# Kernel optimization log

Measured on AMD Instinct MI355X. Metric: run time of the kernel, lower is better.

## Reference

```python
import jax, jax.numpy as jnp
import numpy as np

N = 100000   # nodes
E = 1600000  # edges (avg degree 16)
F = 128      # num_node_features
H = 128      # hid_size
G = 512      # num graphs in batch
C = 10       # num_classes
D = 32       # graph_degree_distribution.shape[1]
BN_EPS = 1e-5


def setup_inputs() -> dict:
    key = jax.random.key(0)
    ks = jax.random.split(key, 16)
    p = lambda k, shp: jax.random.normal(k, shp, jnp.float32) * 0.02
    x = jax.random.normal(ks[0], (N, F), jnp.float32)
    edge_index = jax.random.randint(ks[1], (2, E), 0, N)
    batch = jnp.sort(jax.random.randint(ks[2], (N,), 0, G))
    degree = jax.random.uniform(ks[3], (N,), jnp.float32) * 10.0
    return dict(
        x=x, edge_index=edge_index, batch=batch, degree=degree,
        eps1=jnp.zeros(()), W1a=p(ks[4], (F, H)), b1a=jnp.zeros(H), W1b=p(ks[5], (H, H)), b1b=jnp.zeros(H),
        g1=jnp.ones(H), be1=jnp.zeros(H),
        eps2=jnp.zeros(()), W2a=p(ks[6], (H, H)), b2a=jnp.zeros(H), W2b=p(ks[7], (H, H)), b2b=jnp.zeros(H),
        g2=jnp.ones(H), be2=jnp.zeros(H),
        Wlin1=p(ks[8], (H, H)), blin1=jnp.zeros(H),
        Wlin2=p(ks[9], (H, C)), blin2=jnp.zeros(C),
        Wlin4=p(ks[10], (H, D)), blin4=jnp.zeros(D),
        Wloss=p(ks[11], (H, 1)), bloss=jnp.zeros(1),
    )


def gin_conv(x, src, dst, eps, Wa, ba, Wb, bb, gamma, beta):
    # GINConv: MLP((1+eps)*x_i + sum_{j->i} x_j); MLP = Lin-ReLU-Lin-ReLU-BN
    agg = jax.ops.segment_sum(x[src], dst, num_segments=x.shape[0])  # [N,F] gather-scatter
    h = (1.0 + eps) * x + agg
    h = jax.nn.relu(h @ Wa + ba)
    h = jax.nn.relu(h @ Wb + bb)
    mu = h.mean(0)
    var = h.var(0)  # biased var, training-mode BN
    return gamma * (h - mu) * jax.lax.rsqrt(var + BN_EPS) + beta


def reference(x, edge_index, batch, degree,
              eps1, W1a, b1a, W1b, b1b, g1, be1,
              eps2, W2a, b2a, W2b, b2b, g2, be2,
              Wlin1, blin1, Wlin2, blin2, Wlin4, blin4, Wloss, bloss):
    src, dst = edge_index[0], edge_index[1]
    h = gin_conv(x, src, dst, eps1, W1a, b1a, W1b, b1b, g1, be1)
    h = gin_conv(h, src, dst, eps2, W2a, b2a, W2b, b2b, g2, be2)
    mse_x = h @ Wloss + bloss                       # [N,1]
    mse_loss = jnp.mean((mse_x - degree[:, None]) ** 2)
    # global_mean_pool over graphs
    sums = jax.ops.segment_sum(h, batch, num_segments=G)
    cnts = jax.ops.segment_sum(jnp.ones((h.shape[0], 1), h.dtype), batch, num_segments=G)
    g = sums / jnp.maximum(cnts, 1.0)               # [G,H]
    z = jax.nn.relu(g @ Wlin1 + blin1)              # dropout inert (eval)
    result1 = jax.nn.log_softmax(z @ Wlin2 + blin2, axis=-1)  # [G,C]
    result3 = z @ Wlin4 + blin4                      # [G,D]
    return result1, result3, mse_loss
```

## Files before the change

kernel.cpp:

```cpp
#include <hip/hip_runtime.h>
#include <hip/hip_bf16.h>

#define HF 128
#define BSH 8
#define BSZ 256
#define NBMAX 1024
#define FCAP 8192
#define HB 512

typedef __attribute__((ext_vector_type(8))) short bf16x8;
typedef __attribute__((ext_vector_type(4))) float f32x4;
typedef __attribute__((ext_vector_type(2))) float f32x2;

__device__ inline float bflo(unsigned u) { return __uint_as_float(u << 16); }
__device__ inline float bfhi(unsigned u) { return __uint_as_float(u & 0xffff0000u); }
__device__ inline unsigned short f2bf(float f) {
    unsigned u = __float_as_uint(f);
    unsigned r = (u + 0x7fffu + ((u >> 16) & 1u)) >> 16;
    return (unsigned short)r;
}
__device__ inline unsigned pack2(float a, float b) {
    return (unsigned)f2bf(a) | ((unsigned)f2bf(b) << 16);
}
__device__ inline uint2 pk8_fp8(const float* v) {
    int a = __builtin_amdgcn_cvt_pk_fp8_f32(v[0], v[1], 0, 0);
    a = __builtin_amdgcn_cvt_pk_fp8_f32(v[2], v[3], a, 1);
    int b = __builtin_amdgcn_cvt_pk_fp8_f32(v[4], v[5], 0, 0);
    b = __builtin_amdgcn_cvt_pk_fp8_f32(v[6], v[7], b, 1);
    uint2 r; r.x = (unsigned)a; r.y = (unsigned)b;
    return r;
}

__global__ __launch_bounds__(256) void init_all(
    const float* __restrict__ x, unsigned short* __restrict__ xb,
    unsigned char* __restrict__ x8, int castBlk, int nchunks,
    const float* __restrict__ w0, const float* __restrict__ w1,
    const float* __restrict__ w2, const float* __restrict__ w3,
    unsigned short* __restrict__ WtAll,
    const int* __restrict__ dst, int* __restrict__ bpart, int E, int chunkH,
    const int* __restrict__ batch, int* __restrict__ gstart, int N, int Gn, int nBlocks,
    float* __restrict__ Szero, float* __restrict__ outm)
{
    __shared__ int lh[NBMAX];
    int b = blockIdx.x;
    int t = threadIdx.x;
    if (b < castBlk) {
        int i = b * 256 + t;
        if (i < nchunks) {
            float4 a = ((const float4*)x)[2 * i];
            float4 c = ((const float4*)x)[2 * i + 1];
            uint4 o;
            o.x = pack2(a.x, a.y); o.y = pack2(a.z, a.w);
            o.z = pack2(c.x, c.y); o.w = pack2(c.z, c.w);
            ((uint4*)xb)[i] = o;
            float v[8] = {a.x, a.y, a.z, a.w, c.x, c.y, c.z, c.w};
            ((uint2*)x8)[i] = pk8_fp8(v);
        }
        return;
    }
    b -= castBlk;
    if (b < 4) {
        const float* W = (b == 0) ? w0 : (b == 1) ? w1 : (b == 2) ? w2 : w3;
        unsigned short* O = WtAll + b * 16384;
        for (int idx = t; idx < 16384; idx += 256) {
            int j    = idx & 7;
            int lane = (idx >> 3) & 63;
            int fk   = idx >> 9;
            int kk = fk & 3, nt = fk >> 2;
            int m = lane & 15, quad = lane >> 4;
            int ncol = nt * 16 + m;
            int krow = kk * 32 + quad * 8 + j;
            O[idx] = f2bf(W[krow * 128 + ncol]);
        }
        return;
    }
    b -= 4;
    if (b < HB) {
        int NBl = (N + BSZ - 1) >> BSH;
        for (int i = t; i < NBl; i += 256) lh[i] = 0;
        __syncthreads();
        int beg = b * chunkH;
        int end = min(E, beg + chunkH);
        for (int e = beg + t; e < end; e += 256)
            atomicAdd(&lh[dst[e] >> BSH], 1);
        __syncthreads();
        for (int i = t; i < NBl; i += 256) bpart[i * HB + b] = lh[i];
        return;
    }
    b -= HB;
    if (b < nBlocks) {
        int i = b * 256 + t;
        if (i >= N) return;
        int bi = batch[i];
        int bp = (i == 0) ? -1 : batch[i - 1];
        for (int g = bp + 1; g <= bi; g++) gstart[g] = i;
        if (i == N - 1)
            for (int g = bi + 1; g <= Gn; g++) gstart[g] = N;
        return;
    }
    if (t < 2 * HF) { Szero[t] = 0.f; Szero[t + 2 * HF] = 0.f; }
    if (t == 0) outm[0] = 0.f;
}

__global__ void scanp(const int* __restrict__ bpart, int* __restrict__ boff,
                      int* __restrict__ bcur, int NB, int E)
{
    __shared__ int tot[NBMAX];
    __shared__ int part[256];
    int t = threadIdx.x;
    for (int i = t; i < NB; i += 256) {
        const int4* pp = (const int4*)(bpart + (size_t)i * HB);
        int run = 0;
#pragma unroll 4
        for (int b = 0; b < HB / 4; b++) {
            int4 v = pp[b];
            run += v.x + v.y + v.z + v.w;
        }
        tot[i] = run;
    }
    __syncthreads();
    int v[4];
    int s = 0;
#pragma unroll
    for (int i = 0; i < 4; i++) {
        int idx = t * 4 + i;
        v[i] = (idx < NB) ? tot[idx] : 0;
        s += v[i];
    }
    part[t] = s;
    __syncthreads();
    for (int o = 1; o < 256; o <<= 1) {
        int y = (t >= o) ? part[t - o] : 0;
        __syncthreads();
        part[t] += y;
        __syncthreads();
    }
    int base = part[t] - s;
#pragma unroll
    for (int i = 0; i < 4; i++) {
        int idx = t * 4 + i;
        if (idx < NB) { boff[idx] = base; bcur[idx] = base; base += v[i]; }
    }
    if (t == 0) boff[NB] = E;
}

__global__ __launch_bounds__(256) void bucket_bin(
    const int* __restrict__ src, const int* __restrict__ dst,
    int* __restrict__ bcur, unsigned* __restrict__ ebuf, int E, int NB, int chunkH)
{
    __shared__ int lh[NBMAX];
    int t = threadIdx.x;
    for (int i = t; i < NB; i += 256) lh[i] = 0;
    __syncthreads();
    int beg = blockIdx.x * chunkH;
    int end = min(E, beg + chunkH);
    for (int e = beg + t; e < end; e += 256)
        atomicAdd(&lh[dst[e] >> BSH], 1);
    __syncthreads();
    for (int i = t; i < NB; i += 256) {
        int c = lh[i];
        lh[i] = c ? atomicAdd(&bcur[i], c) : 0;
    }
    __syncthreads();
    for (int e = beg + t; e < end; e += 256) {
        int d = dst[e];
        int b = d >> BSH;
        int pos = atomicAdd(&lh[b], 1);
        ebuf[pos] = ((unsigned)src[e] << BSH) | (unsigned)(d & (BSZ - 1));
    }
}

__global__ __launch_bounds__(256) void bucket_fill(
    const unsigned* __restrict__ ebuf, const int* __restrict__ boff,
    int* __restrict__ off, int* __restrict__ esrc, int N, int NB, int E)
{
    __shared__ int deg[BSZ];
    __shared__ int pref[BSZ];
    __shared__ int lcur[BSZ];
    __shared__ int lsr[FCAP];
    int b = blockIdx.x;
    int t = threadIdx.x;
    int segBeg = boff[b], segEnd = boff[b + 1];
    int segLen = segEnd - segBeg;
    int node0 = b << BSH;
    deg[t] = 0;
    __syncthreads();
    for (int i = segBeg + t; i < segEnd; i += 256)
        atomicAdd(&deg[ebuf[i] & (BSZ - 1)], 1);
    __syncthreads();
    int dv = deg[t];
    pref[t] = dv;
    __syncthreads();
    for (int o = 1; o < 256; o <<= 1) {
        int y = (t >= o) ? pref[t - o] : 0;
        __syncthreads();
        pref[t] += y;
        __syncthreads();
    }
    int excl = pref[t] - dv;
    int node = node0 + t;
    if (node < N) off[node] = segBeg + excl;
    lcur[t] = excl;
    if (b == NB - 1 && t == 0) off[N] = E;
    __syncthreads();
    if (segLen <= FCAP) {
        for (int i = segBeg + t; i < segEnd; i += 256) {
            unsigned v = ebuf[i];
            int slot = atomicAdd(&lcur[v & (BSZ - 1)], 1);
            lsr[slot] = (int)(v >> BSH);
        }
        __syncthreads();
        for (int i = t; i < segLen; i += 256) esrc[segBeg + i] = lsr[i];
    } else {
        for (int i = segBeg + t; i < segEnd; i += 256) {
            unsigned v = ebuf[i];
            int slot = atomicAdd(&lcur[v & (BSZ - 1)], 1);
            esrc[segBeg + slot] = (int)(v >> BSH);
        }
    }
}

template <bool FOLD>
__global__ __launch_bounds__(256) void gather_u(
    const unsigned short* __restrict__ xb, const unsigned char* __restrict__ x8,
    const int* __restrict__ off, const int* __restrict__ esrc,
    const float* __restrict__ epsp,
    const float* __restrict__ S1, const float* __restrict__ S2,
    const float* __restrict__ gamma, const float* __restrict__ beta, float invN,
    unsigned short* __restrict__ Uo, int N)
{
    __shared__ float lsc[HF], lsh[HF];
    int tid = threadIdx.x;
    if (FOLD) {
        if (tid < HF) {
            float mu = S1[tid] * invN;
            float var = S2[tid] * invN - mu * mu;
            float rs = rsqrtf(var + 1e-5f);
            float sc = gamma[tid] * rs;
            lsc[tid] = sc;
            lsh[tid] = beta[tid] - mu * sc;
        }
        __syncthreads();
    }
    int lane16 = tid & 15;
    int node = (blockIdx.x * 256 + tid) >> 4;
    if (node >= N) return;
    int beg = off[node], end = off[node + 1];
    float acc[8] = {0.f, 0.f, 0.f, 0.f, 0.f, 0.f, 0.f, 0.f};
    for (int j0 = beg; j0 < end; j0 += 16) {
        int myidx = (j0 + lane16 < end) ? esrc[j0 + lane16] : 0;
        int cnt = min(16, end - j0);
        for (int t = 0; t < cnt; t++) {
            int s = __shfl(myidx, t, 16);
            uint2 p = *(const uint2*)(x8 + (size_t)s * HF + lane16 * 8);
            f32x2 f0 = __builtin_amdgcn_cvt_pk_f32_fp8((int)p.x, 0);
            f32x2 f1 = __builtin_amdgcn_cvt_pk_f32_fp8((int)p.x, 1);
            f32x2 f2 = __builtin_amdgcn_cvt_pk_f32_fp8((int)p.y, 0);
            f32x2 f3 = __builtin_amdgcn_cvt_pk_f32_fp8((int)p.y, 1);
            acc[0] += f0.x; acc[1] += f0.y;
            acc[2] += f1.x; acc[3] += f1.y;
            acc[4] += f2.x; acc[5] += f2.y;
            acc[6] += f3.x; acc[7] += f3.y;
        }
    }
    float ep = 1.0f + epsp[0];
    uint4 xx = *(const uint4*)(xb + (size_t)node * HF + lane16 * 8);
    acc[0] += ep * bflo(xx.x); acc[1] += ep * bfhi(xx.x);
    acc[2] += ep * bflo(xx.y); acc[3] += ep * bfhi(xx.y);
    acc[4] += ep * bflo(xx.z); acc[5] += ep * bfhi(xx.z);
    acc[6] += ep * bflo(xx.w); acc[7] += ep * bfhi(xx.w);
    if (FOLD) {
        float cf = ep + (float)(end - beg);
        const float4 s0 = *(const float4*)(&lsc[lane16 * 8]);
        const float4 s1 = *(const float4*)(&lsc[lane16 * 8 + 4]);
        const float4 h0 = *(const float4*)(&lsh[lane16 * 8]);
        const float4 h1 = *(const float4*)(&lsh[lane16 * 8 + 4]);
        acc[0] = acc[0] * s0.x + h0.x * cf; acc[1] = acc[1] * s0.y + h0.y * cf;
        acc[2] = acc[2] * s0.z + h0.z * cf; acc[3] = acc[3] * s0.w + h0.w * cf;
        acc[4] = acc[4] * s1.x + h1.x * cf; acc[5] = acc[5] * s1.y + h1.y * cf;
        acc[6] = acc[6] * s1.z + h1.z * cf; acc[7] = acc[7] * s1.w + h1.w * cf;
    }
    uint4 o;
    o.x = pack2(acc[0], acc[1]); o.y = pack2(acc[2], acc[3]);
    o.z = pack2(acc[4], acc[5]); o.w = pack2(acc[6], acc[7]);
    *(uint4*)(Uo + (size_t)node * HF + lane16 * 8) = o;
}

__global__ __launch_bounds__(256) void gemm2L(
    const unsigned short* __restrict__ U,
    const unsigned short* __restrict__ Wfa, const float* __restrict__ ba,
    const unsigned short* __restrict__ Wfb, const float* __restrict__ bb,
    unsigned short* __restrict__ out, unsigned char* __restrict__ out8,
    float* __restrict__ S1, float* __restrict__ S2, int n)
{
    __shared__ __align__(16) unsigned short lWa[16384];
    __shared__ __align__(16) unsigned short lWb[16384];
    __shared__ __align__(16) unsigned short lT[8192];
    int tid = threadIdx.x;
    int w = tid >> 6, lane = tid & 63;
    int m = lane & 15, quad = lane >> 4;

    for (int i = tid; i < 2048; i += 256) {
        ((uint4*)lWa)[i] = ((const uint4*)Wfa)[i];
        ((uint4*)lWb)[i] = ((const uint4*)Wfb)[i];
    }
    __syncthreads();

    float bav[8], bbv[8];
#pragma unroll
    for (int nt = 0; nt < 8; nt++) { bav[nt] = ba[nt * 16 + m]; bbv[nt] = bb[nt * 16 + m]; }

    unsigned short* lTw = lT + w * 2048;
    int swzA = (m & 7) << 3;

    float csA[8], cqA[8];
#pragma unroll
    for (int nt = 0; nt < 8; nt++) { csA[nt] = 0.f; cqA[nt] = 0.f; }

    int wid = (blockIdx.x << 2) | w;
    int nw = gridDim.x << 2;
    int ntiles = (n + 15) >> 4;

    bf16x8 aF[4];
    int tile = wid;
    if (tile < ntiles) {
        int ar = tile * 16 + m; if (ar >= n) ar = n - 1;
        const unsigned short* up = U + (size_t)ar * HF + quad * 8;
#pragma unroll
        for (int kk = 0; kk < 4; kk++) aF[kk] = *(const bf16x8*)(up + kk * 32);
    }

    for (; tile < ntiles; tile += nw) {
        bf16x8 aN[4];
        {
            int tn = tile + nw;
            int tl = (tn < ntiles) ? tn : tile;
            int ar = tl * 16 + m; if (ar >= n) ar = n - 1;
            const unsigned short* up = U + (size_t)ar * HF + quad * 8;
#pragma unroll
            for (int kk = 0; kk < 4; kk++) aN[kk] = *(const bf16x8*)(up + kk * 32);
        }

        f32x4 acc[8];
#pragma unroll
        for (int nt = 0; nt < 8; nt++) acc[nt] = (f32x4){0.f, 0.f, 0.f, 0.f};
#pragma unroll
        for (int nt = 0; nt < 8; nt++) {
#pragma unroll
            for (int kk = 0; kk < 4; kk++) {
                bf16x8 b = *(const bf16x8*)(&lWa[((((nt << 2) | kk) << 6) | lane) << 3]);
                acc[nt] = __builtin_amdgcn_mfma_f32_16x16x32_bf16(aF[kk], b, acc[nt], 0, 0, 0);
            }
        }
#pragma unroll
        for (int nt = 0; nt < 8; nt++) {
#pragma unroll
            for (int r = 0; r < 4; r++) {
                int row = (quad << 2) | r;
                lTw[(row << 7) | ((nt * 16 + m) ^ ((row & 7) << 3))] =
                    f2bf(fmaxf(acc[nt][r] + bav[nt], 0.f));
            }
        }
        bf16x8 a2[4];
#pragma unroll
        for (int kk = 0; kk < 4; kk++)
            a2[kk] = *(const bf16x8*)(&lTw[(m << 7) | (((kk << 5) | (quad << 3)) ^ swzA)]);
#pragma unroll
        for (int nt = 0; nt < 8; nt++) acc[nt] = (f32x4){0.f, 0.f, 0.f, 0.f};
#pragma unroll
        for (int nt = 0; nt < 8; nt++) {
#pragma unroll
            for (int kk = 0; kk < 4; kk++) {
                bf16x8 b = *(const bf16x8*)(&lWb[((((nt << 2) | kk) << 6) | lane) << 3]);
                acc[nt] = __builtin_amdgcn_mfma_f32_16x16x32_bf16(a2[kk], b, acc[nt], 0, 0, 0);
            }
        }
        int row0 = tile << 4;
#pragma unroll
        for (int nt = 0; nt < 8; nt++) {
            float cs = 0.f, cq = 0.f;
#pragma unroll
            for (int r = 0; r < 4; r++) {
                int row = (quad << 2) | r;
                float v = fmaxf(acc[nt][r] + bbv[nt], 0.f);
                lTw[(row << 7) | ((nt * 16 + m) ^ ((row & 7) << 3))] = f2bf(v);
                if (row0 + row < n) { cs += v; cq += v * v; }
            }
            cs += __shfl_down(cs, 32); cs += __shfl_down(cs, 16);
            cq += __shfl_down(cq, 32); cq += __shfl_down(cq, 16);
            csA[nt] += cs; cqA[nt] += cq;
        }
#pragma unroll
        for (int i = 0; i < 4; i++) {
            int chunk = (i << 6) | lane;
            int row = chunk >> 4, c16 = chunk & 15;
            int grow = row0 + row;
            if (grow < n) {
                uint4 v = *(const uint4*)(&lTw[(row << 7) | (((c16 << 3) ^ ((row & 7) << 3)))]);
                *(uint4*)(out + (size_t)grow * HF + (c16 << 3)) = v;
                if (out8) {
                    float f[8] = {bflo(v.x), bfhi(v.x), bflo(v.y), bfhi(v.y),
                                  bflo(v.z), bfhi(v.z), bflo(v.w), bfhi(v.w)};
                    *(uint2*)(out8 + (size_t)grow * HF + (c16 << 3)) = pk8_fp8(f);
                }
            }
        }
#pragma unroll
        for (int kk = 0; kk < 4; kk++) aF[kk] = aN[kk];
    }

    if (quad == 0) {
#pragma unroll
        for (int nt = 0; nt < 8; nt++) {
            atomicAdd(&S1[nt * 16 + m], csA[nt]);
            atomicAdd(&S2[nt * 16 + m], cqA[nt]);
        }
    }
}

__global__ __launch_bounds__(512) void pool_tail(
    const unsigned short* __restrict__ h2raw,
    const float* __restrict__ S1, const float* __restrict__ S2,
    const float* __restrict__ gamma, const float* __restrict__ beta, float invN,
    const int* __restrict__ gstart, const float* __restrict__ W,
    const float* __restrict__ bias,
    const float* __restrict__ Wloss, const float* __restrict__ blossp,
    const float* __restrict__ degree,
    const float* __restrict__ W2, const float* __restrict__ b2,
    const float* __restrict__ W4, const float* __restrict__ b4,
    float* __restrict__ out1, float* __restrict__ out3,
    float* __restrict__ outm, int C_, int D_)
{
    __shared__ float lsc[HF], lsh[HF];
    __shared__ float red[8][HF];
    __shared__ float gv[HF];
    __shared__ float part[4][HF];
    __shared__ float wred[8];
    __shared__ float zz[HF];
    __shared__ float logits[16];
    __shared__ float lse_s;
    int gid = blockIdx.x;
    int t = threadIdx.x;
    if (t < HF) {
        float mu = S1[t] * invN;
        float var = S2[t] * invN - mu * mu;
        float rs = rsqrtf(var + 1e-5f);
        float sc = gamma[t] * rs;
        lsc[t] = sc;
        lsh[t] = beta[t] - mu * sc;
    }
    __syncthreads();
    int c2 = t & 63;
    int rg = t >> 6;
    int b = gstart[gid], e = gstart[gid + 1];
    float wla = lsc[2 * c2] * Wloss[2 * c2];
    float wlb = lsc[2 * c2 + 1] * Wloss[2 * c2 + 1];
    float c0l = lsh[2 * c2] * Wloss[2 * c2] + lsh[2 * c2 + 1] * Wloss[2 * c2 + 1];
    float bl = blossp[0];
    float s0 = 0.f, s1 = 0.f, macc = 0.f;
    for (int r = b + rg; r < e; r += 8) {
        unsigned u = *(const unsigned*)(h2raw + (size_t)r * HF + c2 * 2);
        float v0 = bflo(u), v1 = bfhi(u);
        s0 += v0; s1 += v1;
        float m = v0 * wla + v1 * wlb + c0l;
#pragma unroll
        for (int o = 32; o > 0; o >>= 1) m += __shfl_down(m, o);
        if (c2 == 0) {
            float d = m + bl - degree[r];
            macc += d * d;
        }
    }
    red[rg][c2 * 2] = s0;
    red[rg][c2 * 2 + 1] = s1;
    if (c2 == 0) wred[rg] = macc;
    __syncthreads();
    if (t < HF) {
        float s = red[0][t] + red[1][t] + red[2][t] + red[3][t]
                + red[4][t] + red[5][t] + red[6][t] + red[7][t];
        gv[t] = (e > b) ? lsc[t] * (s / (float)(e - b)) + lsh[t] : 0.f;
    }
    __syncthreads();
    int c = t & 127, kg = t >> 7;
    float a = 0.f;
#pragma unroll 8
    for (int k = kg * 32; k < kg * 32 + 32; k++) a += gv[k] * W[(size_t)k * HF + c];
    part[kg][c] = a;
    __syncthreads();
    if (t < HF) {
        float aa = part[0][t] + part[1][t] + part[2][t] + part[3][t] + bias[t];
        zz[t] = fmaxf(aa, 0.f);
    }
    if (t == 0) {
        float ps = wred[0] + wred[1] + wred[2] + wred[3]
                 + wred[4] + wred[5] + wred[6] + wred[7];
        atomicAdd(outm, ps * invN);
    }
    __syncthreads();
    if (t < C_) {
        float aa = b2[t];
        for (int k = 0; k < HF; k++) aa += zz[k] * W2[(size_t)k * C_ + t];
        logits[t] = aa;
    }
    __syncthreads();
    if (t == 0) {
        float mx = -1e30f;
        for (int i = 0; i < C_; i++) mx = fmaxf(mx, logits[i]);
        float s = 0.f;
        for (int i = 0; i < C_; i++) s += expf(logits[i] - mx);
        lse_s = mx + logf(s);
    }
    __syncthreads();
    if (t < C_) out1[(size_t)gid * C_ + t] = logits[t] - lse_s;
    if (t < D_) {
        float aa = b4[t];
        for (int k = 0; k < HF; k++) aa += zz[k] * W4[(size_t)k * D_ + t];
        out3[(size_t)gid * D_ + t] = aa;
    }
}

extern "C" void kernel_launch(void* const* d_in, const int* in_sizes, int n_in,
                              void* d_out, int out_size, void* d_ws, size_t ws_size,
                              hipStream_t stream)
{
    const float* x      = (const float*)d_in[0];
    const int*   ei     = (const int*)d_in[1];
    const int*   batch  = (const int*)d_in[2];
    const float* degree = (const float*)d_in[3];
    const float* eps1   = (const float*)d_in[4];
    const float* W1a    = (const float*)d_in[5];
    const float* b1a    = (const float*)d_in[6];
    const float* W1b    = (const float*)d_in[7];
    const float* b1b    = (const float*)d_in[8];
    const float* g1     = (const float*)d_in[9];
    const float* be1    = (const float*)d_in[10];
    const float* eps2   = (const float*)d_in[11];
    const float* W2a    = (const float*)d_in[12];
    const float* b2a    = (const float*)d_in[13];
    const float* W2b    = (const float*)d_in[14];
    const float* b2b    = (const float*)d_in[15];
    const float* g2     = (const float*)d_in[16];
    const float* be2    = (const float*)d_in[17];
    const float* Wlin1  = (const float*)d_in[18];
    const float* blin1  = (const float*)d_in[19];
    const float* Wlin2  = (const float*)d_in[20];
    const float* blin2  = (const float*)d_in[21];
    const float* Wlin4  = (const float*)d_in[22];
    const float* blin4  = (const float*)d_in[23];
    const float* Wloss  = (const float*)d_in[24];
    const float* bloss  = (const float*)d_in[25];

    const int N  = in_sizes[0] / HF;
    const int E  = in_sizes[1] / 2;
    const int C_ = in_sizes[21];
    const int D_ = in_sizes[23];
    const int Gn = (out_size - 1) / (C_ + D_);
    const int NB = (N + BSZ - 1) >> BSH;

    const int* src = ei;
    const int* dst = ei + E;

    size_t NH = (size_t)N * HF;
    char* p = (char*)d_ws;
    unsigned short* xb  = (unsigned short*)p; p += NH * 2;
    unsigned short* U   = (unsigned short*)p; p += NH * 2;
    unsigned short* Hp1 = (unsigned short*)p; p += NH * 2;
    unsigned short* Hp2 = (unsigned short*)p; p += NH * 2;
    unsigned char*  x8  = (unsigned char*)p; p += NH;
    unsigned char*  h8  = (unsigned char*)p; p += NH;
    unsigned short* WtAll = (unsigned short*)p; p += 4 * 16384 * 2;
    float* S1a  = (float*)p; p += HF * 4;
    float* S2a  = (float*)p; p += HF * 4;
    float* S1b  = (float*)p; p += HF * 4;
    float* S2b  = (float*)p; p += HF * 4;
    int* gstart = (int*)p; p += (Gn + 1) * 4;
    int* boff   = (int*)p; p += (NBMAX + 1) * 4;
    int* bcur   = (int*)p; p += NBMAX * 4;
    int* bpart  = (int*)p; p += (size_t)NBMAX * HB * 4;
    int* off    = (int*)p; p += (N + 1) * 4;
    int* esrc   = (int*)p; p += E * 4;
    unsigned* ebuf = (unsigned*)p; p += E * 4;

    unsigned short* Wt1a = WtAll;
    unsigned short* Wt1b = WtAll + 16384;
    unsigned short* Wt2a = WtAll + 32768;
    unsigned short* Wt2b = WtAll + 49152;

    float* out1 = (float*)d_out;
    float* out3 = out1 + (size_t)Gn * C_;
    float* outm = out3 + (size_t)Gn * D_;

    int nchunks  = (int)(NH / 8);
    int castBlk  = (nchunks + 255) / 256;
    int nBlocks  = (N + 255) / 256;
    int gatherBlk = (N * 16 + 255) / 256;
    int gemmBlk  = 512;
    int chunkH   = (E + HB - 1) / HB;
    float invN = 1.0f / (float)N;

    int initBlk = castBlk + 4 + HB + nBlocks + 1;

    init_all<<<initBlk, 256, 0, stream>>>(x, xb, x8, castBlk, nchunks,
                                          W1a, W1b, W2a, W2b, WtAll,
                                          dst, bpart, E, chunkH,
                                          batch, gstart, N, Gn, nBlocks,
                                          S1a, outm);
    scanp<<<1, 256, 0, stream>>>(bpart, boff, bcur, NB, E);
    bucket_bin<<<HB, 256, 0, stream>>>(src, dst, bcur, ebuf, E, NB, chunkH);
    bucket_fill<<<NB, 256, 0, stream>>>(ebuf, boff, off, esrc, N, NB, E);
    gather_u<false><<<gatherBlk, 256, 0, stream>>>(xb, x8, off, esrc, eps1,
                                                   nullptr, nullptr, nullptr, nullptr, 0.f, U, N);
    gemm2L<<<gemmBlk, 256, 0, stream>>>(U, Wt1a, b1a, Wt1b, b1b, Hp1, h8, S1a, S2a, N);
    gather_u<true><<<gatherBlk, 256, 0, stream>>>(Hp1, h8, off, esrc, eps2,
                                                  S1a, S2a, g1, be1, invN, U, N);
    gemm2L<<<gemmBlk, 256, 0, stream>>>(U, Wt2a, b2a, Wt2b, b2b, Hp2, nullptr, S1b, S2b, N);
    pool_tail<<<Gn, 512, 0, stream>>>(Hp2, S1b, S2b, g2, be2, invN, gstart,
                                      Wlin1, blin1, Wloss, bloss, degree,
                                      Wlin2, blin2, Wlin4, blin4,
                                      out1, out3, outm, C_, D_);
}
```

Before: 492.0 us.

## Accumulate bucket totals atomically and stream GEMM weights from global per tile

Histogram blocks now add their per-bucket counts straight into a global totals array, zeroed by a memset. This removes the 512-way partial-count matrix that the single-block scan had to sum. The fused two-layer GEMM no longer stages both weight matrices in LDS. It launches one 16-row tile per wave with an occupancy hint, reads weight fragments directly from global memory, and reduces BN statistics through LDS atomics before one global atomic per column per block. This cuts LDS use and the serial scan work, but every wave now re-reads 64KB of weights through the caches, and per-block prologue and atomic overhead grows.

```diff
diff --git a/kernel.cpp b/kernel.cpp
--- a/kernel.cpp
+++ b/kernel.cpp
@@ -37,7 +37,7 @@
     const float* __restrict__ w0, const float* __restrict__ w1,
     const float* __restrict__ w2, const float* __restrict__ w3,
     unsigned short* __restrict__ WtAll,
-    const int* __restrict__ dst, int* __restrict__ bpart, int E, int chunkH,
+    const int* __restrict__ dst, int* __restrict__ tot, int E, int chunkH,
     const int* __restrict__ batch, int* __restrict__ gstart, int N, int Gn, int nBlocks,
     float* __restrict__ Szero, float* __restrict__ outm)
 {
@@ -84,7 +84,10 @@
         for (int e = beg + t; e < end; e += 256)
             atomicAdd(&lh[dst[e] >> BSH], 1);
         __syncthreads();
-        for (int i = t; i < NBl; i += 256) bpart[i * HB + b] = lh[i];
+        for (int i = t; i < NBl; i += 256) {
+            int c = lh[i];
+            if (c) atomicAdd(&tot[i], c);
+        }
         return;
     }
     b -= HB;
@@ -102,23 +105,11 @@
     if (t == 0) outm[0] = 0.f;
 }
 
-__global__ void scanp(const int* __restrict__ bpart, int* __restrict__ boff,
+__global__ void scanp(const int* __restrict__ tot, int* __restrict__ boff,
                       int* __restrict__ bcur, int NB, int E)
 {
-    __shared__ int tot[NBMAX];
     __shared__ int part[256];
     int t = threadIdx.x;
-    for (int i = t; i < NB; i += 256) {
-        const int4* pp = (const int4*)(bpart + (size_t)i * HB);
-        int run = 0;
-#pragma unroll 4
-        for (int b = 0; b < HB / 4; b++) {
-            int4 v = pp[b];
-            run += v.x + v.y + v.z + v.w;
-        }
-        tot[i] = run;
-    }
-    __syncthreads();
     int v[4];
     int s = 0;
 #pragma unroll
@@ -286,60 +277,42 @@
     *(uint4*)(Uo + (size_t)node * HF + lane16 * 8) = o;
 }
 
-__global__ __launch_bounds__(256) void gemm2L(
+__global__ __launch_bounds__(256, 4) void gemm2L(
     const unsigned short* __restrict__ U,
     const unsigned short* __restrict__ Wfa, const float* __restrict__ ba,
     const unsigned short* __restrict__ Wfb, const float* __restrict__ bb,
     unsigned short* __restrict__ out, unsigned char* __restrict__ out8,
     float* __restrict__ S1, float* __restrict__ S2, int n)
 {
-    __shared__ __align__(16) unsigned short lWa[16384];
-    __shared__ __align__(16) unsigned short lWb[16384];
     __shared__ __align__(16) unsigned short lT[8192];
+    __shared__ float lS1[HF], lS2[HF];
     int tid = threadIdx.x;
     int w = tid >> 6, lane = tid & 63;
     int m = lane & 15, quad = lane >> 4;
-
-    for (int i = tid; i < 2048; i += 256) {
-        ((uint4*)lWa)[i] = ((const uint4*)Wfa)[i];
-        ((uint4*)lWb)[i] = ((const uint4*)Wfb)[i];
-    }
-    __syncthreads();
-
-    float bav[8], bbv[8];
-#pragma unroll
-    for (int nt = 0; nt < 8; nt++) { bav[nt] = ba[nt * 16 + m]; bbv[nt] = bb[nt * 16 + m]; }
-
-    unsigned short* lTw = lT + w * 2048;
-    int swzA = (m & 7) << 3;
-
-    float csA[8], cqA[8];
-#pragma unroll
-    for (int nt = 0; nt < 8; nt++) { csA[nt] = 0.f; cqA[nt] = 0.f; }
-
-    int wid = (blockIdx.x << 2) | w;
-    int nw = gridDim.x << 2;
+    int tile = (blockIdx.x << 2) | w;
     int ntiles = (n + 15) >> 4;
-
-    bf16x8 aF[4];
-    int tile = wid;
-    if (tile < ntiles) {
-        int ar = tile * 16 + m; if (ar >= n) ar = n - 1;
+    bool active = tile < ntiles;
+
+    if (tid < HF) { lS1[tid] = 0.f; lS2[tid] = 0.f; }
+    __syncthreads();
+
+    if (active) {
+        unsigned short* lTw = lT + w * 2048;
+        int swzA = (m & 7) << 3;
+        int row0 = tile << 4;
+
+        int ar = row0 + m; if (ar >= n) ar = n - 1;
         const unsigned short* up = U + (size_t)ar * HF + quad * 8;
+        bf16x8 aF[4];
 #pragma unroll
         for (int kk = 0; kk < 4; kk++) aF[kk] = *(const bf16x8*)(up + kk * 32);
-    }
-
-    for (; tile < ntiles; tile += nw) {
-        bf16x8 aN[4];
-        {
-            int tn = tile + nw;
-            int tl = (tn < ntiles) ? tn : tile;
-            int ar = tl * 16 + m; if (ar >= n) ar = n - 1;
-            const unsigned short* up = U + (size_t)ar * HF + quad * 8;
-#pragma unroll
-            for (int kk = 0; kk < 4; kk++) aN[kk] = *(const bf16x8*)(up + kk * 32);
-        }
+
+        float bav[8], bbv[8];
+#pragma unroll
+        for (int nt = 0; nt < 8; nt++) { bav[nt] = ba[nt * 16 + m]; bbv[nt] = bb[nt * 16 + m]; }
+
+        const bf16x8* __restrict__ Ba = (const bf16x8*)Wfa;
+        const bf16x8* __restrict__ Bb = (const bf16x8*)Wfb;
 
         f32x4 acc[8];
 #pragma unroll
@@ -348,7 +321,7 @@
         for (int nt = 0; nt < 8; nt++) {
 #pragma unroll
             for (int kk = 0; kk < 4; kk++) {
-                bf16x8 b = *(const bf16x8*)(&lWa[((((nt << 2) | kk) << 6) | lane) << 3]);
+                bf16x8 b = Ba[(((nt << 2) | kk) << 6) | lane];
                 acc[nt] = __builtin_amdgcn_mfma_f32_16x16x32_bf16(aF[kk], b, acc[nt], 0, 0, 0);
             }
         }
@@ -371,11 +344,10 @@
         for (int nt = 0; nt < 8; nt++) {
 #pragma unroll
             for (int kk = 0; kk < 4; kk++) {
-                bf16x8 b = *(const bf16x8*)(&lWb[((((nt << 2) | kk) << 6) | lane) << 3]);
+                bf16x8 b = Bb[(((nt << 2) | kk) << 6) | lane];
                 acc[nt] = __builtin_amdgcn_mfma_f32_16x16x32_bf16(a2[kk], b, acc[nt], 0, 0, 0);
             }
         }
-        int row0 = tile << 4;
 #pragma unroll
         for (int nt = 0; nt < 8; nt++) {
             float cs = 0.f, cq = 0.f;
@@ -388,7 +360,10 @@
             }
             cs += __shfl_down(cs, 32); cs += __shfl_down(cs, 16);
             cq += __shfl_down(cq, 32); cq += __shfl_down(cq, 16);
-            csA[nt] += cs; cqA[nt] += cq;
+            if (quad == 0) {
+                atomicAdd(&lS1[nt * 16 + m], cs);
+                atomicAdd(&lS2[nt * 16 + m], cq);
+            }
         }
 #pragma unroll
         for (int i = 0; i < 4; i++) {
@@ -405,16 +380,11 @@
                 }
             }
         }
-#pragma unroll
-        for (int kk = 0; kk < 4; kk++) aF[kk] = aN[kk];
-    }
-
-    if (quad == 0) {
-#pragma unroll
-        for (int nt = 0; nt < 8; nt++) {
-            atomicAdd(&S1[nt * 16 + m], csA[nt]);
-            atomicAdd(&S2[nt * 16 + m], cqA[nt]);
-        }
+    }
+    __syncthreads();
+    if (tid < HF) {
+        atomicAdd(&S1[tid], lS1[tid]);
+        atomicAdd(&S2[tid], lS2[tid]);
     }
 }
 
@@ -575,7 +545,7 @@
     int* gstart = (int*)p; p += (Gn + 1) * 4;
     int* boff   = (int*)p; p += (NBMAX + 1) * 4;
     int* bcur   = (int*)p; p += NBMAX * 4;
-    int* bpart  = (int*)p; p += (size_t)NBMAX * HB * 4;
+    int* tot    = (int*)p; p += NBMAX * 4;
     int* off    = (int*)p; p += (N + 1) * 4;
     int* esrc   = (int*)p; p += E * 4;
     unsigned* ebuf = (unsigned*)p; p += E * 4;
@@ -593,18 +563,20 @@
     int castBlk  = (nchunks + 255) / 256;
     int nBlocks  = (N + 255) / 256;
     int gatherBlk = (N * 16 + 255) / 256;
-    int gemmBlk  = 512;
+    int ntiles   = (N + 15) / 16;
+    int gemmBlk  = (ntiles + 3) / 4;
     int chunkH   = (E + HB - 1) / HB;
     float invN = 1.0f / (float)N;
 
     int initBlk = castBlk + 4 + HB + nBlocks + 1;
 
+    hipMemsetAsync(tot, 0, (size_t)NB * sizeof(int), stream);
     init_all<<<initBlk, 256, 0, stream>>>(x, xb, x8, castBlk, nchunks,
                                           W1a, W1b, W2a, W2b, WtAll,
-                                          dst, bpart, E, chunkH,
+                                          dst, tot, E, chunkH,
                                           batch, gstart, N, Gn, nBlocks,
                                           S1a, outm);
-    scanp<<<1, 256, 0, stream>>>(bpart, boff, bcur, NB, E);
+    scanp<<<1, 256, 0, stream>>>(tot, boff, bcur, NB, E);
     bucket_bin<<<HB, 256, 0, stream>>>(src, dst, bcur, ebuf, E, NB, chunkH);
     bucket_fill<<<NB, 256, 0, stream>>>(ebuf, boff, off, esrc, N, NB, E);
     gather_u<false><<<gatherBlk, 256, 0, stream>>>(xb, x8, off, esrc, eps1,
```

Result: faster. 479.2 us (-2.6%).
